# Kernel tuning notes

Measured on AMD Instinct MI355X. Metric: run time of the kernel, lower is better.

The kernel has to match this reference:

```python
import jax, jax.numpy as jnp
import numpy as np

N_NODES, N_EDGES, N_GRAPHS = 20000, 640000, 256
D_IN, H1, H2, H3, L, H4, ED = 7, 128, 128, 64, 16, 64, 1


def _gat_conv(x, src, dst, edge_attr, W, att_s, att_d, We, att_e, b):
    """PyG GATConv (heads=1, concat=True, edge_dim=ED, add_self_loops=True,
    fill_value='mean' for self-loop edge attrs, negative_slope=0.2)."""
    n = x.shape[0]
    h = x @ W                                  # [N, F]
    a_s = h @ att_s                            # [N]
    a_d = h @ att_d                            # [N]
    # append self loops; self-loop edge attr = mean of edge attrs
    loop = jnp.arange(n)
    src_f = jnp.concatenate([src, loop])
    dst_f = jnp.concatenate([dst, loop])
    ea_mean = edge_attr.mean(axis=0, keepdims=True)
    ea = jnp.concatenate([edge_attr, jnp.broadcast_to(ea_mean, (n, edge_attr.shape[1]))], axis=0)
    a_e = (ea @ We) @ att_e                    # [E+N]
    logits = jax.nn.leaky_relu(a_s[src_f] + a_d[dst_f] + a_e, 0.2)
    # neighborhood softmax over incoming edges of each dst node
    m = jax.ops.segment_max(logits, dst_f, num_segments=n)
    ex = jnp.exp(logits - m[dst_f])
    denom = jax.ops.segment_sum(ex, dst_f, num_segments=n)
    alpha = ex / denom[dst_f]                  # [E+N]
    out = jax.ops.segment_sum(alpha[:, None] * h[src_f], dst_f, num_segments=n)
    return out + b


def _branch(x, edge_index, edge_col, params):
    src, dst = edge_index[0], edge_index[1]
    for p in params:  # fixed 3 layers
        x = jax.nn.elu(_gat_conv(x, src, dst, edge_col, *p))
        # dropout p=0.2 is identity in eval mode
    return x


def _mean_pool(x, batch, num_graphs):
    s = jax.ops.segment_sum(x, batch, num_segments=num_graphs)
    cnt = jax.ops.segment_sum(jnp.ones((x.shape[0],), x.dtype), batch, num_segments=num_graphs)
    return s / jnp.maximum(cnt, 1.0)[:, None]


def setup_inputs() -> dict:
    key = jax.random.key(0)
    ks = jax.random.split(key, 40)
    inp = {
        "x1": jax.random.normal(ks[0], (N_NODES, D_IN), jnp.float32),
        "x2": jax.random.normal(ks[1], (N_NODES, D_IN), jnp.float32),
        "edge_index1": jax.random.randint(ks[2], (2, N_EDGES), 0, N_NODES),
        "edge_index2": jax.random.randint(ks[3], (2, N_EDGES), 0, N_NODES),
        "batch1": jnp.sort(jax.random.randint(ks[4], (N_NODES,), 0, N_GRAPHS)),
        "batch2": jnp.sort(jax.random.randint(ks[5], (N_NODES,), 0, N_GRAPHS)),
        "x_norm2_1": jax.random.normal(ks[6], (N_GRAPHS, L), jnp.float32),
        "x_norm2_2": jax.random.normal(ks[7], (N_GRAPHS, L), jnp.float32),
        "edge_col1": jax.random.normal(ks[8], (N_EDGES, ED), jnp.float32),
        "edge_col2": jax.random.normal(ks[9], (N_EDGES, ED), jnp.float32),
    }
    dims = [(D_IN, H1), (H1, H2), (H2, H3)]
    k = 10
    for i, (fi, fo) in enumerate(dims, start=1):
        sc = 1.0 / np.sqrt(fi)
        inp[f"W{i}"] = jax.random.normal(ks[k], (fi, fo), jnp.float32) * sc; k += 1
        inp[f"as{i}"] = jax.random.normal(ks[k], (fo,), jnp.float32) * 0.1; k += 1
        inp[f"ad{i}"] = jax.random.normal(ks[k], (fo,), jnp.float32) * 0.1; k += 1
        inp[f"We{i}"] = jax.random.normal(ks[k], (ED, fo), jnp.float32); k += 1
        inp[f"ae{i}"] = jax.random.normal(ks[k], (fo,), jnp.float32) * 0.1; k += 1
        inp[f"b{i}"] = jnp.zeros((fo,), jnp.float32); k += 1
    inp["linW"] = jax.random.normal(ks[k], (H3 + L, H4), jnp.float32) * (1.0 / np.sqrt(H3 + L)); k += 1
    inp["linb"] = jnp.zeros((H4,), jnp.float32)
    return inp


def reference(x1, x2, edge_index1, edge_index2, batch1, batch2, x_norm2_1, x_norm2_2,
              edge_col1, edge_col2,
              W1, as1, ad1, We1, ae1, b1,
              W2, as2, ad2, We2, ae2, b2,
              W3, as3, ad3, We3, ae3, b3,
              linW, linb):
    params = [(W1, as1, ad1, We1, ae1, b1),
              (W2, as2, ad2, We2, ae2, b2),
              (W3, as3, ad3, We3, ae3, b3)]
    h1 = _branch(x1, edge_index1, edge_col1, params)
    h2 = _branch(x2, edge_index2, edge_col2, params)
    g1 = _mean_pool(h1, batch1, N_GRAPHS)
    g2 = _mean_pool(h2, batch2, N_GRAPHS)
    o1 = jnp.concatenate([g1, x_norm2_1], axis=1) @ linW + linb
    o2 = jnp.concatenate([g2, x_norm2_2], axis=1) @ linW + linb
    return (o1, o2)
```

## Files before the change

### kernel.cpp

```cpp
#include <hip/hip_runtime.h>
#include <hip/hip_bf16.h>
#include <hip/hip_fp16.h>

#define N_NODES 20000
#define N_EDGES 640000
#define N_GRAPHS 256
#define NBUCK 313
#define NC 160
#define EPC 4000
#define DCAP 2560
#define CURP 16
#define STAGEN ((size_t)NBUCK*DCAP)

typedef short bf16v __attribute__((ext_vector_type(8)));
typedef float f32x4 __attribute__((ext_vector_type(4)));
typedef float f32x2 __attribute__((ext_vector_type(2)));

__device__ __forceinline__ float leaky02(float x){ return x > 0.f ? x : 0.2f*x; }
__device__ __forceinline__ float eluf(float x){ return x > 0.f ? x : (__expf(x) - 1.f); }
__device__ __forceinline__ unsigned short f2bf(float x){
  __hip_bfloat16 t = __float2bfloat16(x);
  return *reinterpret_cast<unsigned short*>(&t);
}
__device__ __forceinline__ float bflo(unsigned int u){ return __uint_as_float(u << 16); }
__device__ __forceinline__ float bfhi(unsigned int u){ return __uint_as_float(u & 0xffff0000u); }
__device__ __forceinline__ void pkfma(f32x2& acc, f32x2 a, f32x2 b){
  asm volatile("v_pk_fma_f32 %0, %1, %2, %0" : "+v"(acc) : "v"(a), "v"(b));
}

__global__ void init_kernel(int* __restrict__ bcur){
  int i = blockIdx.x*256 + threadIdx.x;
  if (i < 2*NBUCK){
    int b = i / NBUCK, j = i % NBUCK;
    bcur[((size_t)b*NBUCK + j)*CURP] = j*DCAP;
  }
}

__global__ __launch_bounds__(256) void binC_kernel(
    const int* __restrict__ ei0, const int* __restrict__ ei1,
    const float* __restrict__ ec0, const float* __restrict__ ec1,
    int* __restrict__ bcur, uint2* __restrict__ stage, float* __restrict__ part)
{
  int b = blockIdx.y;
  const int* srcp = (b ? ei1 : ei0);
  const int* dstp = srcp + N_EDGES;
  const float* ec = b ? ec1 : ec0;
  int* bcurb = bcur + (size_t)b*NBUCK*CURP;
  uint2* stageb = stage + (size_t)b*STAGEN;
  __shared__ uint2 recs[EPC];
  __shared__ int hist[NBUCK], rbase[NBUCK], rcur[NBUCK];
  int tid = threadIdx.x;
  for (int j = tid; j < NBUCK; j += 256){ hist[j] = 0; rcur[j] = 0; }
  __syncthreads();
  int e0 = blockIdx.x*EPC;
  float v = 0.f;
  for (int r = tid; r < EPC; r += 256){
    int i = e0 + r;
    int d = dstp[i];
    int bk = d >> 6;
    uint2 rec;
    rec.x = (unsigned)srcp[i] | ((unsigned)(d & 63) << 16);
    float e = ec[i];
    v += e;
    rec.y = ((unsigned)f2bf(e) << 16) | (unsigned)bk;
    recs[r] = rec;
    atomicAdd(&hist[bk], 1);
  }
  __syncthreads();
  for (int j = tid; j < NBUCK; j += 256){
    int h = hist[j];
    rbase[j] = h ? atomicAdd(&bcurb[j*CURP], h) : 0;
  }
  __syncthreads();
  for (int r = tid; r < EPC; r += 256){
    uint2 rc = recs[r];
    int bk = (int)(rc.y & 0xFFFFu);
    int p = rbase[bk] + atomicAdd(&rcur[bk], 1);
    if (p < (bk + 1)*DCAP) stageb[p] = rc;
  }
  for (int o = 32; o; o >>= 1) v += __shfl_down(v, o);
  __shared__ float wr[4];
  int lane = tid & 63, wv = tid >> 6;
  if (lane == 0) wr[wv] = v;
  __syncthreads();
  if (tid == 0) part[b*NC + blockIdx.x] = wr[0]+wr[1]+wr[2]+wr[3];
}

__global__ __launch_bounds__(512) void binB_kernel(
    const float* __restrict__ part,
    const int* __restrict__ bat0, const int* __restrict__ bat1,
    const float* __restrict__ We1, const float* __restrict__ ae1,
    const float* __restrict__ We2, const float* __restrict__ ae2,
    const float* __restrict__ We3, const float* __restrict__ ae3,
    int* __restrict__ gb, float* __restrict__ scal)
{
  int b = blockIdx.x;
  int tid = threadIdx.x;
  if (b == 0){
    int wv = tid >> 6, lane = tid & 63;
    if (wv < 3){
      const float* We = wv==0 ? We1 : (wv==1 ? We2 : We3);
      const float* ae = wv==0 ? ae1 : (wv==1 ? ae2 : ae3);
      int F = (wv==2) ? 64 : 128;
      float s = 0.f;
      for (int i = lane; i < F; i += 64) s += We[i]*ae[i];
      for (int o = 32; o; o >>= 1) s += __shfl_down(s, o);
      if (lane == 0) scal[2+wv] = s;
    }
  }
  {
    float s = 0.f;
    for (int i = tid; i < NC; i += 512) s += part[b*NC + i];
    for (int o = 32; o; o >>= 1) s += __shfl_down(s, o);
    __shared__ float fr[8];
    if ((tid & 63) == 0) fr[tid >> 6] = s;
    __syncthreads();
    if (tid == 0){
      float t = 0.f;
      for (int i = 0; i < 8; ++i) t += fr[i];
      scal[b] = t;
    }
  }
  {
    const int* batch = b ? bat1 : bat0;
    int* gbb = gb + b*257;
    if (tid <= N_GRAPHS){
      int g = tid, lo = 0, hi = N_NODES;
      while (lo < hi){ int mid = (lo+hi) >> 1; if (batch[mid] < g) lo = mid+1; else hi = mid; }
      gbb[g] = lo;
    }
  }
}

__global__ __launch_bounds__(256) void binD_kernel(
    const uint2* __restrict__ stage, const int* __restrict__ bcur,
    unsigned* __restrict__ final_, int2* __restrict__ rowp2)
{
  int b = blockIdx.y;
  int g = blockIdx.x;
  int tid = threadIdx.x;
  const uint2* stageb = stage + (size_t)b*STAGEN;
  unsigned* finb = final_ + (size_t)b*STAGEN;
  int2* rowb = rowp2 + (size_t)b*N_NODES;
  int cb = g*DCAP;
  int n = min(bcur[((size_t)b*NBUCK + g)*CURP] - cb, DCAP);
  __shared__ uint2 recs[DCAP];
  __shared__ int cnt64[64], cur64[64], off64[64];
  if (tid < 64) cnt64[tid] = 0;
  __syncthreads();
  for (int r = tid; r < n; r += 256){
    uint2 rc = stageb[cb + r];
    recs[r] = rc;
    atomicAdd(&cnt64[(rc.x >> 16) & 63], 1);
  }
  __syncthreads();
  if (tid == 0){
    int acc = 0;
    for (int dl = 0; dl < 64; ++dl){
      off64[dl] = acc; cur64[dl] = acc; acc += cnt64[dl];
    }
  }
  __syncthreads();
  int nd = min(64, N_NODES - g*64);
  if (tid < nd)
    rowb[g*64 + tid] = make_int2(cb + off64[tid], cb + off64[tid] + cnt64[tid]);
  for (int r = tid; r < n; r += 256){
    uint2 rc = recs[r];
    int dl = (rc.x >> 16) & 63;
    int p = atomicAdd(&cur64[dl], 1);
    finb[cb + p] = (rc.y & 0xFFFF0000u) | (rc.x & 0xFFFFu);
  }
}

template<int K, int F>
__global__ __launch_bounds__(256) void node_linear1_kernel(
    const float* __restrict__ x0, const float* __restrict__ x1,
    const float* __restrict__ W,
    const float* __restrict__ atts, const float* __restrict__ attd,
    unsigned short* __restrict__ hbAll, float* __restrict__ aSAll, float* __restrict__ aDAll)
{
  int b = blockIdx.y;
  const float* x = b ? x1 : x0;
  unsigned short* hb = hbAll + (size_t)b*N_NODES*128;
  float* a_s = aSAll + b*N_NODES;
  float* a_d = aDAll + b*N_NODES;
  constexpr int ROWS = 256 / F;
  __shared__ float Wl[K*F];
  __shared__ float xl[ROWS*K];
  __shared__ float swv[4], dwv[4];
  int tid = threadIdx.x;
  for (int i = tid; i < K*F; i += 256) Wl[i] = W[i];
  int f = tid % F;
  int lr = tid / F;
  float vs = atts[f], vd = attd[f];
  const int ntiles = (N_NODES + ROWS - 1)/ROWS;
  for (int t = blockIdx.x; t < ntiles; t += gridDim.x){
    int r0 = t*ROWS;
    __syncthreads();
    for (int i = tid; i < ROWS*K; i += 256){
      int r = i / K, k = i % K;
      int row = r0 + r;
      xl[i] = (row < N_NODES) ? x[row*K + k] : 0.f;
    }
    __syncthreads();
    float acc = 0.f;
    #pragma unroll
    for (int k = 0; k < K; ++k) acc += xl[lr*K + k] * Wl[k*F + f];
    int row = r0 + lr;
    if (row < N_NODES) hb[row*F + f] = f2bf(acc);
    float s = acc*vs, d = acc*vd;
    #pragma unroll
    for (int o = 32; o; o >>= 1){ s += __shfl_down(s, o); d += __shfl_down(d, o); }
    int wv = tid >> 6;
    if ((tid & 63) == 0){ swv[wv] = s; dwv[wv] = d; }
    __syncthreads();
    if (f == 0 && row < N_NODES){
      a_s[row] = swv[2*lr] + swv[2*lr+1];
      a_d[row] = dwv[2*lr] + dwv[2*lr+1];
    }
  }
}

template<int F>
__global__ __launch_bounds__(256) void gemm_mfma_kernel(
    const unsigned short* __restrict__ AAll, const float* __restrict__ W,
    const float* __restrict__ atts, const float* __restrict__ attd,
    unsigned short* __restrict__ hbAll, float* __restrict__ aSAll, float* __restrict__ aDAll)
{
  int b = blockIdx.y;
  const unsigned short* A = AAll + (size_t)b*N_NODES*128;
  unsigned short* hb = hbAll + (size_t)b*N_NODES*128;
  float* a_s = aSAll + b*N_NODES;
  float* a_d = aDAll + b*N_NODES;
  constexpr int NT = F/16;
  constexpr int KP = 136;
  __shared__ unsigned short Wb[F*KP];
  int tid = threadIdx.x;
  for (int idx = tid; idx < 128*F; idx += 256){
    int k = idx / F, col = idx % F;
    Wb[col*KP + k] = f2bf(W[idx]);
  }
  __syncthreads();
  int wave = tid >> 6, lane = tid & 63;
  int r0w = blockIdx.x*64 + wave*16;
  int arow = r0w + (lane & 15);
  bool av = arow < N_NODES;
  f32x4 acc[NT];
  #pragma unroll
  for (int nt = 0; nt < NT; ++nt) acc[nt] = 0.f;
  #pragma unroll
  for (int step = 0; step < 4; ++step){
    int kbase = step*32 + (lane>>4)*8;
    uint4 araw = av ? *reinterpret_cast<const uint4*>(&A[(size_t)arow*128 + kbase])
                    : make_uint4(0,0,0,0);
    bf16v af = __builtin_bit_cast(bf16v, araw);
    #pragma unroll
    for (int nt = 0; nt < NT; ++nt){
      uint4 braw = *reinterpret_cast<const uint4*>(&Wb[(nt*16 + (lane&15))*KP + kbase]);
      bf16v bfr = __builtin_bit_cast(bf16v, braw);
      acc[nt] = __builtin_amdgcn_mfma_f32_16x16x32_bf16(af, bfr, acc[nt], 0, 0, 0);
    }
  }
  float ps[4] = {0,0,0,0}, pd[4] = {0,0,0,0};
  #pragma unroll
  for (int nt = 0; nt < NT; ++nt){
    int col = nt*16 + (lane&15);
    float vs = atts[col], vd = attd[col];
    #pragma unroll
    for (int reg = 0; reg < 4; ++reg){
      int row = r0w + (lane>>4)*4 + reg;
      float v = acc[nt][reg];
      if (row < N_NODES) hb[(size_t)row*F + col] = f2bf(v);
      ps[reg] += v*vs;
      pd[reg] += v*vd;
    }
  }
  #pragma unroll
  for (int reg = 0; reg < 4; ++reg){
    float s = ps[reg], d = pd[reg];
    #pragma unroll
    for (int o = 1; o < 16; o <<= 1){ s += __shfl_xor(s, o); d += __shfl_xor(d, o); }
    int row = r0w + (lane>>4)*4 + reg;
    if ((lane & 15) == 0 && row < N_NODES){ a_s[row] = s; a_d[row] = d; }
  }
}

template<int F, bool W32>
__global__ __launch_bounds__(256) void aggregate_kernel(
    const unsigned short* __restrict__ hbAll,
    const float* __restrict__ aSAll, const float* __restrict__ aDAll,
    const unsigned* __restrict__ edgAll, const int2* __restrict__ rowp2All,
    const float* __restrict__ scal, int l,
    const float* __restrict__ bias,
    float* __restrict__ out32All, unsigned short* __restrict__ outbAll)
{
  constexpr int PERL = F/16;
  constexpr int PERH = PERL/2;
  constexpr int RSH = (F == 128) ? 8 : 7;
  constexpr int SUBB = (F == 128) ? 16 : 8;
  int bid = blockIdx.x;
  int b = bid & 1;
  const unsigned short* hb = hbAll + (size_t)b*N_NODES*128;
  const float* a_s = aSAll + b*N_NODES;
  const float* a_d = aDAll + b*N_NODES;
  const unsigned* edges = edgAll + (size_t)b*STAGEN;
  const int2* rowp2 = rowp2All + (size_t)b*N_NODES;
  __shared__ uint2 sp[4][64];
  int wv = threadIdx.x >> 6;
  int lane = threadIdx.x & 63;
  int half = lane >> 5;
  int hl = lane & 31;
  int d = (bid >> 1)*8 + wv*2 + half;
  int sub = hl & 15, grp = hl >> 4;
  const char* hb2 = (const char*)hb + sub*SUBB;
  float c = scal[2+l];
  float ae_self = (scal[b] * (1.0f/N_EDGES)) * c;
  float add_ = a_d[d];
  float p_self = __expf(fminf(leaky02(a_s[d] + add_ + ae_self), 60.f));
  float dsum = 0.f;
  f32x2 acc[PERH];
  #pragma unroll
  for (int i = 0; i < PERH; ++i) acc[i] = (f32x2){0.f, 0.f};
  if (grp == 0){
    f32x2 pself2 = {p_self, p_self};
    if (PERL == 8){
      uint4 q = *reinterpret_cast<const uint4*>(hb2 + ((unsigned)d << RSH));
      pkfma(acc[0], (f32x2){bflo(q.x), bfhi(q.x)}, pself2);
      pkfma(acc[1], (f32x2){bflo(q.y), bfhi(q.y)}, pself2);
      pkfma(acc[2], (f32x2){bflo(q.z), bfhi(q.z)}, pself2);
      pkfma(acc[3], (f32x2){bflo(q.w), bfhi(q.w)}, pself2);
    } else {
      uint2 q = *reinterpret_cast<const uint2*>(hb2 + ((unsigned)d << RSH));
      pkfma(acc[0], (f32x2){bflo(q.x), bfhi(q.x)}, pself2);
      pkfma(acc[1], (f32x2){bflo(q.y), bfhi(q.y)}, pself2);
    }
  }
  int2 r2 = rowp2[d];
  int e0 = r2.x, deg = r2.y - r2.x;
  int degmax = max(deg, __shfl_xor(deg, 32));
  for (int ch = 0; ch < degmax; ch += 32){
    int n = deg - ch;
    unsigned off0 = 0;
    float p0 = 0.f;
    if (hl < n){
      unsigned e = edges[e0 + ch + hl];
      unsigned s0 = e & 0xFFFFu;
      p0 = __expf(fminf(leaky02(a_s[s0] + add_ + c*bfhi(e)), 60.f));
      off0 = s0 << RSH;
    }
    dsum += p0;
    sp[wv][lane] = make_uint2(off0, __float_as_uint(p0));
    int nmax = min(32, degmax - ch);
    #pragma unroll 4
    for (int e8 = 0; e8 < nmax; e8 += 8){
      int base = half*32 + e8 + grp;
      uint2 r0 = sp[wv][base];
      uint2 r1 = sp[wv][base + 2];
      uint2 rr2 = sp[wv][base + 4];
      uint2 r3 = sp[wv][base + 6];
      f32x2 a0 = {__uint_as_float(r0.y), __uint_as_float(r0.y)};
      f32x2 a1 = {__uint_as_float(r1.y), __uint_as_float(r1.y)};
      f32x2 a2 = {__uint_as_float(rr2.y), __uint_as_float(rr2.y)};
      f32x2 a3 = {__uint_as_float(r3.y), __uint_as_float(r3.y)};
      if (PERL == 8){
        uint4 q0 = *reinterpret_cast<const uint4*>(hb2 + r0.x);
        uint4 q1 = *reinterpret_cast<const uint4*>(hb2 + r1.x);
        uint4 q2 = *reinterpret_cast<const uint4*>(hb2 + rr2.x);
        uint4 q3 = *reinterpret_cast<const uint4*>(hb2 + r3.x);
        pkfma(acc[0], (f32x2){bflo(q0.x), bfhi(q0.x)}, a0);
        pkfma(acc[1], (f32x2){bflo(q0.y), bfhi(q0.y)}, a0);
        pkfma(acc[2], (f32x2){bflo(q0.z), bfhi(q0.z)}, a0);
        pkfma(acc[3], (f32x2){bflo(q0.w), bfhi(q0.w)}, a0);
        pkfma(acc[0], (f32x2){bflo(q1.x), bfhi(q1.x)}, a1);
        pkfma(acc[1], (f32x2){bflo(q1.y), bfhi(q1.y)}, a1);
        pkfma(acc[2], (f32x2){bflo(q1.z), bfhi(q1.z)}, a1);
        pkfma(acc[3], (f32x2){bflo(q1.w), bfhi(q1.w)}, a1);
        pkfma(acc[0], (f32x2){bflo(q2.x), bfhi(q2.x)}, a2);
        pkfma(acc[1], (f32x2){bflo(q2.y), bfhi(q2.y)}, a2);
        pkfma(acc[2], (f32x2){bflo(q2.z), bfhi(q2.z)}, a2);
        pkfma(acc[3], (f32x2){bflo(q2.w), bfhi(q2.w)}, a2);
        pkfma(acc[0], (f32x2){bflo(q3.x), bfhi(q3.x)}, a3);
        pkfma(acc[1], (f32x2){bflo(q3.y), bfhi(q3.y)}, a3);
        pkfma(acc[2], (f32x2){bflo(q3.z), bfhi(q3.z)}, a3);
        pkfma(acc[3], (f32x2){bflo(q3.w), bfhi(q3.w)}, a3);
      } else {
        uint2 q0 = *reinterpret_cast<const uint2*>(hb2 + r0.x);
        uint2 q1 = *reinterpret_cast<const uint2*>(hb2 + r1.x);
        uint2 q2 = *reinterpret_cast<const uint2*>(hb2 + rr2.x);
        uint2 q3 = *reinterpret_cast<const uint2*>(hb2 + r3.x);
        pkfma(acc[0], (f32x2){bflo(q0.x), bfhi(q0.x)}, a0);
        pkfma(acc[1], (f32x2){bflo(q0.y), bfhi(q0.y)}, a0);
        pkfma(acc[0], (f32x2){bflo(q1.x), bfhi(q1.x)}, a1);
        pkfma(acc[1], (f32x2){bflo(q1.y), bfhi(q1.y)}, a1);
        pkfma(acc[0], (f32x2){bflo(q2.x), bfhi(q2.x)}, a2);
        pkfma(acc[1], (f32x2){bflo(q2.y), bfhi(q2.y)}, a2);
        pkfma(acc[0], (f32x2){bflo(q3.x), bfhi(q3.x)}, a3);
        pkfma(acc[1], (f32x2){bflo(q3.y), bfhi(q3.y)}, a3);
      }
    }
  }
  #pragma unroll
  for (int o = 16; o; o >>= 1) dsum += __shfl_xor(dsum, o);
  float denom = p_self + dsum;
  float inv = 1.0f/denom;
  float vv[PERL];
  #pragma unroll
  for (int i = 0; i < PERH; ++i){
    float v0 = acc[i].x, v1 = acc[i].y;
    v0 += __shfl_xor(v0, 16);
    v1 += __shfl_xor(v1, 16);
    vv[2*i]   = eluf(v0*inv + bias[PERL*sub + 2*i]);
    vv[2*i+1] = eluf(v1*inv + bias[PERL*sub + 2*i+1]);
  }
  if (grp == 0){
    if (W32){
      float* out32 = out32All + (size_t)b*N_NODES*64;
      *reinterpret_cast<float4*>(&out32[(size_t)d*64 + 4*sub]) = make_float4(vv[0],vv[1],vv[2],vv[3]);
    } else {
      unsigned short* outb = outbAll + (size_t)b*N_NODES*128;
      if (PERL == 8){
        uint4 o;
        o.x = (unsigned int)f2bf(vv[0]) | ((unsigned int)f2bf(vv[1]) << 16);
        o.y = (unsigned int)f2bf(vv[2]) | ((unsigned int)f2bf(vv[3]) << 16);
        o.z = (unsigned int)f2bf(vv[4]) | ((unsigned int)f2bf(vv[5]) << 16);
        o.w = (unsigned int)f2bf(vv[6]) | ((unsigned int)f2bf(vv[7]) << 16);
        *reinterpret_cast<uint4*>(&outb[(size_t)d*F + 8*sub]) = o;
      } else {
        uint2 o;
        o.x = (unsigned int)f2bf(vv[0]) | ((unsigned int)f2bf(vv[1]) << 16);
        o.y = (unsigned int)f2bf(vv[2]) | ((unsigned int)f2bf(vv[3]) << 16);
        *reinterpret_cast<uint2*>(&outb[(size_t)d*F + 4*sub]) = o;
      }
    }
  }
}

__global__ __launch_bounds__(256) void pool_final_kernel(
    const float* __restrict__ buf0, const int* __restrict__ gb,
    const float* __restrict__ xn0, const float* __restrict__ xn1,
    const float* __restrict__ linW, const float* __restrict__ linb,
    float* __restrict__ out)
{
  int bg = blockIdx.x;
  int b = bg >> 8, g = bg & 255;
  __shared__ float Wl[80*64];
  __shared__ float red[4][64];
  __shared__ float mf[64];
  int tid = threadIdx.x;
  for (int i = tid; i < 80*64; i += 256) Wl[i] = linW[i];
  const float* x = buf0 + (size_t)b*N_NODES*64;
  const int* gbb = gb + b*257;
  int s = gbb[g], e = gbb[g+1];
  int f = tid & 63, rg = tid >> 6;
  float acc = 0.f;
  for (int r = s + rg; r < e; r += 4) acc += x[r*64 + f];
  red[rg][f] = acc;
  __syncthreads();
  if (rg == 0)
    mf[f] = (red[0][f]+red[1][f]+red[2][f]+red[3][f]) / fmaxf((float)(e - s), 1.0f);
  __syncthreads();
  if (tid < 64){
    int j = tid;
    const float* xn = b ? xn1 : xn0;
    float a2 = linb[j];
    #pragma unroll 8
    for (int k = 0; k < 64; ++k) a2 += mf[k] * Wl[k*64 + j];
    #pragma unroll
    for (int k = 0; k < 16; ++k) a2 += xn[g*16+k] * Wl[(64+k)*64 + j];
    out[(size_t)(b*N_GRAPHS + g)*64 + j] = a2;
  }
}

extern "C" void kernel_launch(void* const* d_in, const int* in_sizes, int n_in,
                              void* d_out, int out_size, void* d_ws, size_t ws_size,
                              hipStream_t stream)
{
  const float* x1   = (const float*)d_in[0];
  const float* x2   = (const float*)d_in[1];
  const int*   ei1  = (const int*)d_in[2];
  const int*   ei2  = (const int*)d_in[3];
  const int*   bat1 = (const int*)d_in[4];
  const int*   bat2 = (const int*)d_in[5];
  const float* xn1  = (const float*)d_in[6];
  const float* xn2  = (const float*)d_in[7];
  const float* ec1  = (const float*)d_in[8];
  const float* ec2  = (const float*)d_in[9];
  const float* W[3]   = {(const float*)d_in[10], (const float*)d_in[16], (const float*)d_in[22]};
  const float* as_[3] = {(const float*)d_in[11], (const float*)d_in[17], (const float*)d_in[23]};
  const float* ad_[3] = {(const float*)d_in[12], (const float*)d_in[18], (const float*)d_in[24]};
  const float* We[3]  = {(const float*)d_in[13], (const float*)d_in[19], (const float*)d_in[25]};
  const float* ae[3]  = {(const float*)d_in[14], (const float*)d_in[20], (const float*)d_in[26]};
  const float* bb[3]  = {(const float*)d_in[15], (const float*)d_in[21], (const float*)d_in[27]};
  const float* linW = (const float*)d_in[28];
  const float* linb = (const float*)d_in[29];
  float* out = (float*)d_out;

  char* ws = (char*)d_ws;
  size_t off = 0;
  auto alloc = [&](size_t bytes)->char*{
    char* p = ws + off;
    off = (off + bytes + 255) & ~(size_t)255;
    return p;
  };
  unsigned short* hbA = (unsigned short*)alloc((size_t)2*N_NODES*128*2);
  unsigned short* hbB = (unsigned short*)alloc((size_t)2*N_NODES*128*2);
  float* buf0 = (float*)alloc((size_t)2*N_NODES*64*4);
  float* aS   = (float*)alloc((size_t)2*N_NODES*4);
  float* aD   = (float*)alloc((size_t)2*N_NODES*4);
  int* bcur   = (int*)alloc((size_t)2*NBUCK*CURP*4);
  int2* rowp2 = (int2*)alloc((size_t)2*N_NODES*8);
  uint2* stage = (uint2*)alloc((size_t)2*STAGEN*8);
  unsigned* final_ = (unsigned*)alloc((size_t)2*STAGEN*4);
  float* part = (float*)alloc((size_t)2*NC*4);
  int* gb     = (int*)alloc((size_t)2*257*4);
  float* scal = (float*)alloc(64);

  init_kernel<<<(2*NBUCK + 255)/256, 256, 0, stream>>>(bcur);
  binC_kernel<<<dim3(NC,2), 256, 0, stream>>>(ei1, ei2, ec1, ec2, bcur, stage, part);
  binB_kernel<<<2, 512, 0, stream>>>(part, bat1, bat2,
      We[0], ae[0], We[1], ae[1], We[2], ae[2], gb, scal);
  binD_kernel<<<dim3(NBUCK,2), 256, 0, stream>>>(stage, bcur, final_, rowp2);

  const int AGG = 2*(N_NODES/8);

  node_linear1_kernel<7,128><<<dim3(1024,2), 256, 0, stream>>>(
      x1, x2, W[0], as_[0], ad_[0], hbA, aS, aD);
  aggregate_kernel<128,false><<<AGG, 256, 0, stream>>>(
      hbA, aS, aD, final_, rowp2, scal, 0, bb[0], nullptr, hbB);

  gemm_mfma_kernel<128><<<dim3((N_NODES+63)/64,2), 256, 0, stream>>>(
      hbB, W[1], as_[1], ad_[1], hbA, aS, aD);
  aggregate_kernel<128,false><<<AGG, 256, 0, stream>>>(
      hbA, aS, aD, final_, rowp2, scal, 1, bb[1], nullptr, hbB);

  gemm_mfma_kernel<64><<<dim3((N_NODES+63)/64,2), 256, 0, stream>>>(
      hbB, W[2], as_[2], ad_[2], hbA, aS, aD);
  aggregate_kernel<64,true><<<AGG, 256, 0, stream>>>(
      hbA, aS, aD, final_, rowp2, scal, 2, bb[2], buf0, nullptr);

  pool_final_kernel<<<2*N_GRAPHS, 256, 0, stream>>>(
      buf0, gb, xn1, xn2, linW, linb, out);
}
```

Baseline: 188.4 us.

## Merge setup kernels, prefetch edge records in aggregate, store final layer as bf16

Folds the bucket-cursor init, graph-boundary search and edge-attention scalars into one setup kernel. The edge-sum reduction moves into binD, which removes the binB launch. The aggregate loop now loads the next chunk's edge record and the a_s gather ahead of use to hide latency. The last layer writes bf16 instead of fp32, and pooling reads bf16. This lowers the launch count and memory traffic, at the cost of slightly lower precision in the final layer output and extra clamped speculative loads.

```diff
diff --git a/kernel.cpp b/kernel.cpp
--- a/kernel.cpp
+++ b/kernel.cpp
@@ -24,15 +24,41 @@
 }
 __device__ __forceinline__ float bflo(unsigned int u){ return __uint_as_float(u << 16); }
 __device__ __forceinline__ float bfhi(unsigned int u){ return __uint_as_float(u & 0xffff0000u); }
+__device__ __forceinline__ float bfs(unsigned short u){ return __uint_as_float(((unsigned)u) << 16); }
 __device__ __forceinline__ void pkfma(f32x2& acc, f32x2 a, f32x2 b){
   asm volatile("v_pk_fma_f32 %0, %1, %2, %0" : "+v"(acc) : "v"(a), "v"(b));
 }
 
-__global__ void init_kernel(int* __restrict__ bcur){
-  int i = blockIdx.x*256 + threadIdx.x;
-  if (i < 2*NBUCK){
-    int b = i / NBUCK, j = i % NBUCK;
-    bcur[((size_t)b*NBUCK + j)*CURP] = j*DCAP;
+__global__ __launch_bounds__(512) void setup_kernel(
+    const int* __restrict__ bat0, const int* __restrict__ bat1,
+    const float* __restrict__ We1, const float* __restrict__ ae1,
+    const float* __restrict__ We2, const float* __restrict__ ae2,
+    const float* __restrict__ We3, const float* __restrict__ ae3,
+    int* __restrict__ bcur, int* __restrict__ gb, float* __restrict__ scal)
+{
+  int b = blockIdx.x;
+  int tid = threadIdx.x;
+  if (tid < NBUCK) bcur[((size_t)b*NBUCK + tid)*CURP] = tid*DCAP;
+  {
+    const int* batch = b ? bat1 : bat0;
+    int* gbb = gb + b*257;
+    if (tid <= N_GRAPHS){
+      int g = tid, lo = 0, hi = N_NODES;
+      while (lo < hi){ int mid = (lo+hi) >> 1; if (batch[mid] < g) lo = mid+1; else hi = mid; }
+      gbb[g] = lo;
+    }
+  }
+  if (b == 0){
+    int wv = tid >> 6, lane = tid & 63;
+    if (wv < 3){
+      const float* We = wv==0 ? We1 : (wv==1 ? We2 : We3);
+      const float* ae = wv==0 ? ae1 : (wv==1 ? ae2 : ae3);
+      int F = (wv==2) ? 64 : 128;
+      float s = 0.f;
+      for (int i = lane; i < F; i += 64) s += We[i]*ae[i];
+      for (int o = 32; o; o >>= 1) s += __shfl_down(s, o);
+      if (lane == 0) scal[2+wv] = s;
+    }
   }
 }
 
@@ -86,59 +112,23 @@
   if (tid == 0) part[b*NC + blockIdx.x] = wr[0]+wr[1]+wr[2]+wr[3];
 }
 
-__global__ __launch_bounds__(512) void binB_kernel(
-    const float* __restrict__ part,
-    const int* __restrict__ bat0, const int* __restrict__ bat1,
-    const float* __restrict__ We1, const float* __restrict__ ae1,
-    const float* __restrict__ We2, const float* __restrict__ ae2,
-    const float* __restrict__ We3, const float* __restrict__ ae3,
-    int* __restrict__ gb, float* __restrict__ scal)
-{
-  int b = blockIdx.x;
-  int tid = threadIdx.x;
-  if (b == 0){
-    int wv = tid >> 6, lane = tid & 63;
-    if (wv < 3){
-      const float* We = wv==0 ? We1 : (wv==1 ? We2 : We3);
-      const float* ae = wv==0 ? ae1 : (wv==1 ? ae2 : ae3);
-      int F = (wv==2) ? 64 : 128;
-      float s = 0.f;
-      for (int i = lane; i < F; i += 64) s += We[i]*ae[i];
-      for (int o = 32; o; o >>= 1) s += __shfl_down(s, o);
-      if (lane == 0) scal[2+wv] = s;
-    }
-  }
-  {
-    float s = 0.f;
-    for (int i = tid; i < NC; i += 512) s += part[b*NC + i];
-    for (int o = 32; o; o >>= 1) s += __shfl_down(s, o);
-    __shared__ float fr[8];
-    if ((tid & 63) == 0) fr[tid >> 6] = s;
-    __syncthreads();
-    if (tid == 0){
-      float t = 0.f;
-      for (int i = 0; i < 8; ++i) t += fr[i];
-      scal[b] = t;
-    }
-  }
-  {
-    const int* batch = b ? bat1 : bat0;
-    int* gbb = gb + b*257;
-    if (tid <= N_GRAPHS){
-      int g = tid, lo = 0, hi = N_NODES;
-      while (lo < hi){ int mid = (lo+hi) >> 1; if (batch[mid] < g) lo = mid+1; else hi = mid; }
-      gbb[g] = lo;
-    }
-  }
-}
-
 __global__ __launch_bounds__(256) void binD_kernel(
     const uint2* __restrict__ stage, const int* __restrict__ bcur,
-    unsigned* __restrict__ final_, int2* __restrict__ rowp2)
+    const float* __restrict__ part,
+    unsigned* __restrict__ final_, int2* __restrict__ rowp2, float* __restrict__ scal)
 {
   int b = blockIdx.y;
   int g = blockIdx.x;
   int tid = threadIdx.x;
+  if (g == 0){
+    float s = 0.f;
+    for (int i = tid; i < NC; i += 256) s += part[b*NC + i];
+    for (int o = 32; o; o >>= 1) s += __shfl_down(s, o);
+    __shared__ float fr[4];
+    if ((tid & 63) == 0) fr[tid >> 6] = s;
+    __syncthreads();
+    if (tid == 0) scal[b] = fr[0]+fr[1]+fr[2]+fr[3];
+  }
   const uint2* stageb = stage + (size_t)b*STAGEN;
   unsigned* finb = final_ + (size_t)b*STAGEN;
   int2* rowb = rowp2 + (size_t)b*N_NODES;
@@ -285,14 +275,14 @@
   }
 }
 
-template<int F, bool W32>
+template<int F>
 __global__ __launch_bounds__(256) void aggregate_kernel(
     const unsigned short* __restrict__ hbAll,
     const float* __restrict__ aSAll, const float* __restrict__ aDAll,
     const unsigned* __restrict__ edgAll, const int2* __restrict__ rowp2All,
     const float* __restrict__ scal, int l,
     const float* __restrict__ bias,
-    float* __restrict__ out32All, unsigned short* __restrict__ outbAll)
+    unsigned short* __restrict__ outbAll)
 {
   constexpr int PERL = F/16;
   constexpr int PERH = PERL/2;
@@ -338,14 +328,17 @@
   int2 r2 = rowp2[d];
   int e0 = r2.x, deg = r2.y - r2.x;
   int degmax = max(deg, __shfl_xor(deg, 32));
+  const int cap = (int)STAGEN - 1;
+  unsigned eRec = edges[min(e0 + hl, cap)];
   for (int ch = 0; ch < degmax; ch += 32){
     int n = deg - ch;
+    unsigned eNext = edges[min(e0 + ch + 32 + hl, cap)];
+    unsigned s0 = eRec & 0xFFFFu;
+    float aval = a_s[s0];
     unsigned off0 = 0;
     float p0 = 0.f;
     if (hl < n){
-      unsigned e = edges[e0 + ch + hl];
-      unsigned s0 = e & 0xFFFFu;
-      p0 = __expf(fminf(leaky02(a_s[s0] + add_ + c*bfhi(e)), 60.f));
+      p0 = __expf(fminf(leaky02(aval + add_ + c*bfhi(eRec)), 60.f));
       off0 = s0 << RSH;
     }
     dsum += p0;
@@ -398,6 +391,7 @@
         pkfma(acc[1], (f32x2){bflo(q3.y), bfhi(q3.y)}, a3);
       }
     }
+    eRec = eNext;
   }
   #pragma unroll
   for (int o = 16; o; o >>= 1) dsum += __shfl_xor(dsum, o);
@@ -413,30 +407,25 @@
     vv[2*i+1] = eluf(v1*inv + bias[PERL*sub + 2*i+1]);
   }
   if (grp == 0){
-    if (W32){
-      float* out32 = out32All + (size_t)b*N_NODES*64;
-      *reinterpret_cast<float4*>(&out32[(size_t)d*64 + 4*sub]) = make_float4(vv[0],vv[1],vv[2],vv[3]);
+    unsigned short* outb = outbAll + (size_t)b*N_NODES*F;
+    if (PERL == 8){
+      uint4 o;
+      o.x = (unsigned int)f2bf(vv[0]) | ((unsigned int)f2bf(vv[1]) << 16);
+      o.y = (unsigned int)f2bf(vv[2]) | ((unsigned int)f2bf(vv[3]) << 16);
+      o.z = (unsigned int)f2bf(vv[4]) | ((unsigned int)f2bf(vv[5]) << 16);
+      o.w = (unsigned int)f2bf(vv[6]) | ((unsigned int)f2bf(vv[7]) << 16);
+      *reinterpret_cast<uint4*>(&outb[(size_t)d*F + 8*sub]) = o;
     } else {
-      unsigned short* outb = outbAll + (size_t)b*N_NODES*128;
-      if (PERL == 8){
-        uint4 o;
-        o.x = (unsigned int)f2bf(vv[0]) | ((unsigned int)f2bf(vv[1]) << 16);
-        o.y = (unsigned int)f2bf(vv[2]) | ((unsigned int)f2bf(vv[3]) << 16);
-        o.z = (unsigned int)f2bf(vv[4]) | ((unsigned int)f2bf(vv[5]) << 16);
-        o.w = (unsigned int)f2bf(vv[6]) | ((unsigned int)f2bf(vv[7]) << 16);
-        *reinterpret_cast<uint4*>(&outb[(size_t)d*F + 8*sub]) = o;
-      } else {
-        uint2 o;
-        o.x = (unsigned int)f2bf(vv[0]) | ((unsigned int)f2bf(vv[1]) << 16);
-        o.y = (unsigned int)f2bf(vv[2]) | ((unsigned int)f2bf(vv[3]) << 16);
-        *reinterpret_cast<uint2*>(&outb[(size_t)d*F + 4*sub]) = o;
-      }
+      uint2 o;
+      o.x = (unsigned int)f2bf(vv[0]) | ((unsigned int)f2bf(vv[1]) << 16);
+      o.y = (unsigned int)f2bf(vv[2]) | ((unsigned int)f2bf(vv[3]) << 16);
+      *reinterpret_cast<uint2*>(&outb[(size_t)d*F + 4*sub]) = o;
     }
   }
 }
 
 __global__ __launch_bounds__(256) void pool_final_kernel(
-    const float* __restrict__ buf0, const int* __restrict__ gb,
+    const unsigned short* __restrict__ buf, const int* __restrict__ gb,
     const float* __restrict__ xn0, const float* __restrict__ xn1,
     const float* __restrict__ linW, const float* __restrict__ linb,
     float* __restrict__ out)
@@ -448,12 +437,12 @@
   __shared__ float mf[64];
   int tid = threadIdx.x;
   for (int i = tid; i < 80*64; i += 256) Wl[i] = linW[i];
-  const float* x = buf0 + (size_t)b*N_NODES*64;
+  const unsigned short* x = buf + (size_t)b*N_NODES*64;
   const int* gbb = gb + b*257;
   int s = gbb[g], e = gbb[g+1];
   int f = tid & 63, rg = tid >> 6;
   float acc = 0.f;
-  for (int r = s + rg; r < e; r += 4) acc += x[r*64 + f];
+  for (int r = s + rg; r < e; r += 4) acc += bfs(x[(size_t)r*64 + f]);
   red[rg][f] = acc;
   __syncthreads();
   if (rg == 0)
@@ -504,7 +493,6 @@
   };
   unsigned short* hbA = (unsigned short*)alloc((size_t)2*N_NODES*128*2);
   unsigned short* hbB = (unsigned short*)alloc((size_t)2*N_NODES*128*2);
-  float* buf0 = (float*)alloc((size_t)2*N_NODES*64*4);
   float* aS   = (float*)alloc((size_t)2*N_NODES*4);
   float* aD   = (float*)alloc((size_t)2*N_NODES*4);
   int* bcur   = (int*)alloc((size_t)2*NBUCK*CURP*4);
@@ -515,29 +503,28 @@
   int* gb     = (int*)alloc((size_t)2*257*4);
   float* scal = (float*)alloc(64);
 
-  init_kernel<<<(2*NBUCK + 255)/256, 256, 0, stream>>>(bcur);
+  setup_kernel<<<2, 512, 0, stream>>>(bat1, bat2,
+      We[0], ae[0], We[1], ae[1], We[2], ae[2], bcur, gb, scal);
   binC_kernel<<<dim3(NC,2), 256, 0, stream>>>(ei1, ei2, ec1, ec2, bcur, stage, part);
-  binB_kernel<<<2, 512, 0, stream>>>(part, bat1, bat2,
-      We[0], ae[0], We[1], ae[1], We[2], ae[2], gb, scal);
-  binD_kernel<<<dim3(NBUCK,2), 256, 0, stream>>>(stage, bcur, final_, rowp2);
+  binD_kernel<<<dim3(NBUCK,2), 256, 0, stream>>>(stage, bcur, part, final_, rowp2, scal);
 
   const int AGG = 2*(N_NODES/8);
 
   node_linear1_kernel<7,128><<<dim3(1024,2), 256, 0, stream>>>(
       x1, x2, W[0], as_[0], ad_[0], hbA, aS, aD);
-  aggregate_kernel<128,false><<<AGG, 256, 0, stream>>>(
-      hbA, aS, aD, final_, rowp2, scal, 0, bb[0], nullptr, hbB);
+  aggregate_kernel<128><<<AGG, 256, 0, stream>>>(
+      hbA, aS, aD, final_, rowp2, scal, 0, bb[0], hbB);
 
   gemm_mfma_kernel<128><<<dim3((N_NODES+63)/64,2), 256, 0, stream>>>(
       hbB, W[1], as_[1], ad_[1], hbA, aS, aD);
-  aggregate_kernel<128,false><<<AGG, 256, 0, stream>>>(
-      hbA, aS, aD, final_, rowp2, scal, 1, bb[1], nullptr, hbB);
+  aggregate_kernel<128><<<AGG, 256, 0, stream>>>(
+      hbA, aS, aD, final_, rowp2, scal, 1, bb[1], hbB);
 
   gemm_mfma_kernel<64><<<dim3((N_NODES+63)/64,2), 256, 0, stream>>>(
       hbB, W[2], as_[2], ad_[2], hbA, aS, aD);
-  aggregate_kernel<64,true><<<AGG, 256, 0, stream>>>(
-      hbA, aS, aD, final_, rowp2, scal, 2, bb[2], buf0, nullptr);
+  aggregate_kernel<64><<<AGG, 256, 0, stream>>>(
+      hbA, aS, aD, final_, rowp2, scal, 2, bb[2], hbB);
 
   pool_final_kernel<<<2*N_GRAPHS, 256, 0, stream>>>(
-      buf0, gb, xn1, xn2, linW, linb, out);
-}
+      hbB, gb, xn1, xn2, linW, linb, out);
+}
```

After: 180.8 us. 1.04x faster.
